# Performance work log

Measured on AMD Instinct MI355X. Metric: run time of the kernel, lower is better.

The kernel has to match this reference:

```python
import jax, jax.numpy as jnp
import numpy as np

NUM_ITER = 3
NUM_SLOTS = 8
INPUT_SIZE = 256
SLOT_SIZE = 256
MLP_HIDDEN = 512
HEADS = 4
EPSILON = 1e-8
LN_EPS = 1e-5


def _ln(x, g, b):
    m = jnp.mean(x, axis=-1, keepdims=True)
    v = jnp.mean((x - m) ** 2, axis=-1, keepdims=True)
    return (x - m) * jax.lax.rsqrt(v + LN_EPS) * g + b


def setup_inputs() -> dict:
    key = jax.random.key(0)
    ks = jax.random.split(key, 16)
    B, Nkv, Nq = 64, 1024, NUM_SLOTS
    S, D, Hm = SLOT_SIZE, INPUT_SIZE, MLP_HIDDEN
    def w(k, shape, fan_in):
        return jax.random.normal(k, shape, jnp.float32) * (fan_in ** -0.5)
    return {
        "inputs": jax.random.normal(ks[0], (B, Nkv, D), jnp.float32),
        "slots": jax.random.normal(ks[1], (B, Nq, S), jnp.float32),
        "ln_in_g": jnp.ones((D,), jnp.float32), "ln_in_b": jnp.zeros((D,), jnp.float32),
        "ln_sl_g": jnp.ones((S,), jnp.float32), "ln_sl_b": jnp.zeros((S,), jnp.float32),
        "ln_mlp_g": jnp.ones((S,), jnp.float32), "ln_mlp_b": jnp.zeros((S,), jnp.float32),
        "Wq": w(ks[2], (S, S), S),
        "Wk": w(ks[3], (D, S), D),
        "Wv": w(ks[4], (D, S), D),
        "gru_w_ih": w(ks[5], (3 * S, S), S),
        "gru_w_hh": w(ks[6], (3 * S, S), S),
        "gru_b_ih": jnp.zeros((3 * S,), jnp.float32),
        "gru_b_hh": jnp.zeros((3 * S,), jnp.float32),
        "mlp_w1": w(ks[7], (S, Hm), S),
        "mlp_b1": jnp.zeros((Hm,), jnp.float32),
        "mlp_w2": w(ks[8], (Hm, S), Hm),
        "mlp_b2": jnp.zeros((S,), jnp.float32),
    }


def reference(inputs, slots, ln_in_g, ln_in_b, ln_sl_g, ln_sl_b, ln_mlp_g, ln_mlp_b,
              Wq, Wk, Wv, gru_w_ih, gru_w_hh, gru_b_ih, gru_b_hh,
              mlp_w1, mlp_b1, mlp_w2, mlp_b2):
    B, Nkv, _ = inputs.shape
    _, Nq, S = slots.shape
    H = HEADS
    hd = S // H

    x = _ln(inputs, ln_in_g, ln_in_b)
    k = (x @ Wk).reshape(B, Nkv, H, hd).transpose(0, 2, 1, 3)  # [B,H,Nkv,hd]
    v = (x @ Wv).reshape(B, Nkv, H, hd).transpose(0, 2, 1, 3)  # [B,H,Nkv,hd]
    k = k * (hd ** -0.5)

    attn_vis = None
    for _ in range(NUM_ITER):
        slots_prev = slots
        s = _ln(slots, ln_sl_g, ln_sl_b)
        q = (s @ Wq).reshape(B, Nq, H, hd).transpose(0, 2, 1, 3)  # [B,H,Nq,hd]
        # logits [B,H,Nkv,Nq]
        logits = jnp.einsum('bhnd,bhqd->bhnq', k, q)
        # softmax over (heads * slots) jointly, per kv token
        flat = logits.transpose(0, 2, 1, 3).reshape(B, Nkv, H * Nq)
        attn = jax.nn.softmax(flat, axis=-1).reshape(B, Nkv, H, Nq).transpose(0, 2, 1, 3)
        attn_vis = attn.sum(axis=1).swapaxes(1, 2)  # [B,Nq,Nkv]
        attn = attn + EPSILON
        attn = attn / jnp.sum(attn, axis=-2, keepdims=True)  # normalize over Nkv
        updates = jnp.einsum('bhnq,bhnd->bqhd', attn, v).reshape(B, Nq, S)

        # GRU cell (torch gate order: r, z, n)
        xg = updates.reshape(-1, S) @ gru_w_ih.T + gru_b_ih
        hprev = slots_prev.reshape(-1, S)
        hg = hprev @ gru_w_hh.T + gru_b_hh
        xr, xz, xn = jnp.split(xg, 3, axis=-1)
        hr, hz, hn = jnp.split(hg, 3, axis=-1)
        r = jax.nn.sigmoid(xr + hr)
        z = jax.nn.sigmoid(xz + hz)
        n = jnp.tanh(xn + r * hn)
        h = (1.0 - z) * n + z * hprev
        slots = h.reshape(B, Nq, S)

        m = _ln(slots, ln_mlp_g, ln_mlp_b)
        slots = slots + (jax.nn.relu(m @ mlp_w1 + mlp_b1) @ mlp_w2 + mlp_b2)

    return slots, jax.lax.stop_gradient(attn_vis)
```

## Files before the change

### kernel.cpp

```cpp
#include <hip/hip_runtime.h>
#include <hip/hip_bf16.h>
#include <math.h>

#define EPS_  1e-8f
#define LNEPS 1e-5f

typedef __attribute__((ext_vector_type(8))) short   short8;
typedef __attribute__((ext_vector_type(8))) __bf16  bf16x8;
typedef __attribute__((ext_vector_type(4))) float   f32x4;
typedef unsigned short ushort_t;

__device__ __forceinline__ float bf2f(unsigned int u) { return __uint_as_float(u << 16); }
__device__ __forceinline__ unsigned short f2bf(float f) {
    unsigned int u = __float_as_uint(f);
    u += 0x7fff + ((u >> 16) & 1);
    return (unsigned short)(u >> 16);
}
__device__ __forceinline__ unsigned int cvt_pk_bf16(float lo, float hi) {
    unsigned int r;
    asm("v_cvt_pk_bf16_f32 %0, %1, %2" : "=v"(r) : "v"(lo), "v"(hi));
    return r;
}
__device__ __forceinline__ f32x4 mfma_bf16(short8 a, short8 b, f32x4 c) {
    union U { short8 s; bf16x8 b; };
    U ua, ub; ua.s = a; ub.s = b;
    return __builtin_amdgcn_mfma_f32_16x16x32_bf16(ua.b, ub.b, c, 0, 0, 0);
}
__device__ __forceinline__ float wred_sum(float v) {
#pragma unroll
    for (int off = 32; off > 0; off >>= 1) v += __shfl_xor(v, off);
    return v;
}

__global__ __launch_bounds__(256) void prepack_w_kernel(const float* __restrict__ Wk,
                                                        const float* __restrict__ Wv,
                                                        ushort_t* __restrict__ Wt) {
    int n = blockIdx.x;
    int k = threadIdx.x;
    float v = (n < 256) ? Wk[(size_t)k * 256 + n] * 0.125f : Wv[(size_t)k * 256 + (n - 256)];
    Wt[(size_t)n * 256 + k] = f2bf(v);
}

__global__ __launch_bounds__(256) void prepack_wtp_kernel(const ushort_t* __restrict__ Wt,
                                                          ushort_t* __restrict__ Wtp) {
    int bs = blockIdx.x;
    int wv = bs >> 3, s = bs & 7;
    int ni = threadIdx.x >> 6, l = threadIdx.x & 63;
    int n  = wv * 64 + ni * 16 + (l & 15);
    int k0 = s * 32 + (l >> 4) * 8;
    short8 v = *(const short8*)(Wt + (size_t)n * 256 + k0);
    *(short8*)(Wtp + ((size_t)bs * 4 + ni) * 512 + l * 8) = v;
}

__global__ __launch_bounds__(512) void prepack_slotw_kernel(const float* __restrict__ w_ih,
                                                            const float* __restrict__ w_hh,
                                                            const float* __restrict__ w1,
                                                            const float* __restrict__ w2,
                                                            const float* __restrict__ Wq,
                                                            ushort_t* __restrict__ wg,
                                                            ushort_t* __restrict__ w1p,
                                                            ushort_t* __restrict__ w2q,
                                                            ushort_t* __restrict__ Wqp) {
    int t = threadIdx.x, bid = blockIdx.x, sec = blockIdx.y;
    if (sec == 0) {
        if (bid < 256) {
            int k = bid, c = t & 255;
            const float* src = (t >> 8) ? w_hh : w_ih;
            size_t o = ((size_t)k * 512 + t) * 4;
            wg[o + 0] = f2bf(src[(size_t)(0 * 256 + c) * 256 + k]);
            wg[o + 1] = f2bf(src[(size_t)(1 * 256 + c) * 256 + k]);
            wg[o + 2] = f2bf(src[(size_t)(2 * 256 + c) * 256 + k]);
            wg[o + 3] = 0;
        }
    } else if (sec == 1) {
        if (bid < 64) {
            size_t o = ((size_t)bid * 512 + t) * 4;
#pragma unroll
            for (int i = 0; i < 4; i++) w1p[o + i] = f2bf(w1[(size_t)(bid * 4 + i) * 512 + t]);
        }
    } else if (sec == 2) {
        if (bid < 64) {
            int k4g = bid * 2 + (t >> 8), c = t & 255;
            size_t o = ((size_t)k4g * 256 + c) * 4;
#pragma unroll
            for (int i = 0; i < 4; i++) w2q[o + i] = f2bf(w2[(size_t)(k4g * 4 + i) * 256 + c]);
        }
    } else {
        if (bid < 32) {
            int k4g = bid * 2 + (t >> 8), c = t & 255;
            size_t o = ((size_t)k4g * 256 + c) * 4;
#pragma unroll
            for (int i = 0; i < 4; i++) Wqp[o + i] = f2bf(Wq[(size_t)(k4g * 4 + i) * 256 + c]);
        }
    }
}

__global__ __launch_bounds__(512, 4) void kvproj_mfma_kernel(const float* __restrict__ in,
                                                             const float* __restrict__ g,
                                                             const float* __restrict__ bb,
                                                             const ushort_t* __restrict__ Wtp,
                                                             ushort_t* __restrict__ kvout) {
    __shared__ __align__(16) ushort_t As[64 * 256];
    const int tid = threadIdx.x;
    const int wv = tid >> 6, l = tid & 63;
    const int kc = l >> 4, lr = l & 15;
    const int m0 = blockIdx.x * 64;

    float4 g4 = *(const float4*)(g + l * 4);
    float4 b4 = *(const float4*)(bb + l * 4);
    float4 xv[8];
#pragma unroll
    for (int i = 0; i < 8; i++)
        xv[i] = *(const float4*)(in + (size_t)(m0 + i * 8 + wv) * 256 + l * 4);
#pragma unroll
    for (int i = 0; i < 8; i++) {
        float s1 = xv[i].x + xv[i].y + xv[i].z + xv[i].w;
        float s2 = xv[i].x * xv[i].x + xv[i].y * xv[i].y + xv[i].z * xv[i].z + xv[i].w * xv[i].w;
        s1 = wred_sum(s1);
        s2 = wred_sum(s2);
        float m = s1 * (1.0f / 256.0f);
        float r = rsqrtf(s2 * (1.0f / 256.0f) - m * m + LNEPS);
        float v0 = (xv[i].x - m) * r * g4.x + b4.x;
        float v1 = (xv[i].y - m) * r * g4.y + b4.y;
        float v2 = (xv[i].z - m) * r * g4.z + b4.z;
        float v3 = (xv[i].w - m) * r * g4.w + b4.w;
        uint2 pk = {cvt_pk_bf16(v0, v1), cvt_pk_bf16(v2, v3)};
        int row = i * 8 + wv;
        *(uint2*)&As[row * 256 + (((l >> 1) ^ (row & 15)) * 8) + (l & 1) * 4] = pk;
    }
    __syncthreads();

    f32x4 zero = {0.f, 0.f, 0.f, 0.f};
    f32x4 acc[4][4];
#pragma unroll
    for (int i = 0; i < 4; i++)
#pragma unroll
        for (int jj = 0; jj < 4; jj++) acc[i][jj] = zero;

    const ushort_t* wbase = Wtp + ((size_t)(wv * 8) * 4) * 512 + l * 8;
    short8 bcur[4], bnxt[4];
#pragma unroll
    for (int ni = 0; ni < 4; ni++) bcur[ni] = *(const short8*)(wbase + ni * 512);

#pragma unroll
    for (int s = 0; s < 8; s++) {
        if (s < 7) {
            const ushort_t* wpb = wbase + (size_t)(s + 1) * 4 * 512;
#pragma unroll
            for (int ni = 0; ni < 4; ni++) bnxt[ni] = *(const short8*)(wpb + ni * 512);
        }
        short8 af[4];
#pragma unroll
        for (int mi = 0; mi < 4; mi++) {
            int r2 = lr + mi * 16;
            int c = s * 4 + kc;
            af[mi] = *(const short8*)&As[r2 * 256 + ((c ^ (r2 & 15)) * 8)];
        }
#pragma unroll
        for (int mi = 0; mi < 4; mi++)
#pragma unroll
            for (int ni = 0; ni < 4; ni++)
                acc[mi][ni] = mfma_bf16(af[mi], bcur[ni], acc[mi][ni]);
        if (s < 7) {
#pragma unroll
            for (int ni = 0; ni < 4; ni++) bcur[ni] = bnxt[ni];
        }
    }

    const int odd = l & 1;
    const int colbase = wv * 64;
#pragma unroll
    for (int mi = 0; mi < 4; mi++)
#pragma unroll
        for (int ni = 0; ni < 4; ni++) {
            float s0 = odd ? acc[mi][ni][0] : acc[mi][ni][2];
            float s1_ = odd ? acc[mi][ni][1] : acc[mi][ni][3];
            float r0 = __shfl_xor(s0, 1);
            float r1_ = __shfl_xor(s1_, 1);
            int col0 = colbase + ni * 16 + (lr & ~1);
            unsigned int packA, packB;
            int rowA;
            if (!odd) {
                packA = cvt_pk_bf16(acc[mi][ni][0], r0);
                packB = cvt_pk_bf16(acc[mi][ni][1], r1_);
                rowA = m0 + mi * 16 + kc * 4 + 0;
            } else {
                packA = cvt_pk_bf16(r0, acc[mi][ni][2]);
                packB = cvt_pk_bf16(r1_, acc[mi][ni][3]);
                rowA = m0 + mi * 16 + kc * 4 + 2;
            }
            *(unsigned int*)(kvout + (size_t)rowA * 512 + col0) = packA;
            *(unsigned int*)(kvout + (size_t)(rowA + 1) * 512 + col0) = packB;
        }
}

__global__ __launch_bounds__(256) void qproj_kernel(const float* __restrict__ slots,
                                                    const float* __restrict__ g,
                                                    const float* __restrict__ bvec,
                                                    const float* __restrict__ Wq,
                                                    float* __restrict__ qp) {
    int row = blockIdx.x;
    int tid = threadIdx.x;
    __shared__ float s_s[256];
    __shared__ float red[8];
    float x = slots[(size_t)row * 256 + tid];
    float s1 = wred_sum(x);
    float s2 = wred_sum(x * x);
    if ((tid & 63) == 0) { red[tid >> 6] = s1; red[4 + (tid >> 6)] = s2; }
    __syncthreads();
    float m  = (red[0] + red[1] + red[2] + red[3]) * (1.0f / 256.0f);
    float e2 = (red[4] + red[5] + red[6] + red[7]) * (1.0f / 256.0f);
    float rst = rsqrtf(e2 - m * m + LNEPS);
    s_s[tid] = (x - m) * rst * g[tid] + bvec[tid];
    __syncthreads();
    float acc = 0.f;
#pragma unroll 4
    for (int d = 0; d < 256; d++) acc += s_s[d] * Wq[(size_t)d * 256 + tid];
    int b = row >> 3, q = row & 7;
    qp[((size_t)(b * 4 + (tid >> 6)) * 8 + q) * 64 + (tid & 63)] = acc;
}

__global__ __launch_bounds__(256) void attn_fused_kernel(const ushort_t* __restrict__ kv,
                                                         const float* __restrict__ qp,
                                                         float* __restrict__ Upart,
                                                         float* __restrict__ Cpart,
                                                         float* __restrict__ vis,
                                                         int write_vis) {
    int b = blockIdx.y;
    int chunk = blockIdx.x;
    int tid = threadIdx.x;
    __shared__ __align__(16) ushort_t qfrag[16 * 512];
    __shared__ float att[128][32];
    __shared__ float ubuf[2][2048];
    __shared__ float cred[8][32];

    {
        const float* qb_ = qp + (size_t)b * 2048;
#pragma unroll
        for (int snt = 0; snt < 16; snt++) {
            int s = snt >> 1, nt = snt & 1;
#pragma unroll
            for (int rep = 0; rep < 2; rep++) {
                int idx = tid + rep * 256;
                int k  = s * 32 + ((idx >> 7) << 3) + (idx & 7);
                int hq = nt * 16 + ((idx >> 3) & 15);
                float v = ((k >> 6) == (hq >> 3))
                              ? qb_[(hq >> 3) * 512 + (hq & 7) * 64 + (k & 63)] : 0.f;
                qfrag[snt * 512 + idx] = f2bf(v);
            }
        }
    }
    __syncthreads();

    const int w = tid >> 6, l = tid & 63;
    const int lr = l & 15, kc8 = (l >> 4) * 8;

    short8 qb2[2][8];
#pragma unroll
    for (int s = 0; s < 8; s++) {
        qb2[0][s] = *(const short8*)&qfrag[(s * 2 + 0) * 512 + l * 8];
        qb2[1][s] = *(const short8*)&qfrag[(s * 2 + 1) * 512 + l * 8];
    }
    f32x4 zero = {0.f, 0.f, 0.f, 0.f};
#pragma unroll
    for (int mi_loc = 0; mi_loc < 2; mi_loc++) {
        int mi = w * 2 + mi_loc;
        f32x4 a0 = zero, a1 = zero;
        const ushort_t* abase = kv + (size_t)(b * 1024 + chunk * 128 + mi * 16 + lr) * 512 + kc8;
#pragma unroll
        for (int s = 0; s < 8; s++) {
            short8 af = *(const short8*)(abase + s * 32);
            a0 = mfma_bf16(af, qb2[0][s], a0);
            a1 = mfma_bf16(af, qb2[1][s], a1);
        }
        int row0 = mi * 16 + (l >> 4) * 4;
#pragma unroll
        for (int r = 0; r < 4; r++) {
            att[row0 + r][lr]      = a0[r];
            att[row0 + r][16 + lr] = a1[r];
        }
    }
    __syncthreads();

    {
        int token = tid >> 1, half = tid & 1;
        float v[16];
        float mx = -3.4e38f;
#pragma unroll
        for (int j = 0; j < 16; j++) { v[j] = att[token][half * 16 + j]; mx = fmaxf(mx, v[j]); }
        mx = fmaxf(mx, __shfl_xor(mx, 1));
        float sm = 0.f;
#pragma unroll
        for (int j = 0; j < 16; j++) { v[j] = __expf(v[j] - mx); sm += v[j]; }
        sm += __shfl_xor(sm, 1);
        float inv = 1.0f / sm;
#pragma unroll
        for (int j = 0; j < 16; j++) { v[j] *= inv; att[token][half * 16 + j] = v[j] + EPS_; }
        if (write_vis) {
#pragma unroll
            for (int q = 0; q < 8; q++) {
                float pv = v[q] + v[q + 8];
                float pf = pv + __shfl_xor(pv, 1);
                if (half == 0) vis[(size_t)(b * 8 + q) * 1024 + chunk * 128 + token] = pf;
            }
        }
    }
    __syncthreads();

    {
        int hq2 = tid & 31, grp = tid >> 5;
        float s = 0.f;
#pragma unroll
        for (int i = 0; i < 16; i++) s += att[grp * 16 + i][hq2];
        cred[grp][hq2] = s;
    }
    __syncthreads();
    if (tid < 32) {
        float s = 0.f;
#pragma unroll
        for (int g2 = 0; g2 < 8; g2++) s += cred[g2][tid];
        Cpart[(size_t)(b * 8 + chunk) * 32 + tid] = s;
    }

    const int h_u = l >> 4, d4 = l & 15;
    const int uo = h_u * 64 + d4 * 4;
    float U[8][4];
#pragma unroll
    for (int q = 0; q < 8; q++)
#pragma unroll
        for (int d = 0; d < 4; d++) U[q][d] = 0.f;
    const ushort_t* vbase = kv + (size_t)(b * 1024 + chunk * 128 + w * 32) * 512 + 256 + uo;
    for (int i = 0; i < 32; ++i) {
        uint2 vp = *(const uint2*)(vbase + (size_t)i * 512);
        float v0 = bf2f(vp.x & 0xffffu), v1 = bf2f(vp.x >> 16);
        float v2 = bf2f(vp.y & 0xffffu), v3 = bf2f(vp.y >> 16);
        const float* arow = &att[w * 32 + i][h_u * 8];
        float4 a01 = *(const float4*)(arow);
        float4 a23 = *(const float4*)(arow + 4);
        float aq[8] = {a01.x, a01.y, a01.z, a01.w, a23.x, a23.y, a23.z, a23.w};
#pragma unroll
        for (int q = 0; q < 8; q++) {
            U[q][0] += aq[q] * v0; U[q][1] += aq[q] * v1;
            U[q][2] += aq[q] * v2; U[q][3] += aq[q] * v3;
        }
    }
    if (w & 1) {
        float* dst = ubuf[w >> 1];
#pragma unroll
        for (int q = 0; q < 8; q++) {
            float4 uq = {U[q][0], U[q][1], U[q][2], U[q][3]};
            *(float4*)(dst + q * 256 + uo) = uq;
        }
    }
    __syncthreads();
    if (!(w & 1)) {
        const float* src = ubuf[w >> 1];
#pragma unroll
        for (int q = 0; q < 8; q++) {
            float4 uq = *(const float4*)(src + q * 256 + uo);
            U[q][0] += uq.x; U[q][1] += uq.y; U[q][2] += uq.z; U[q][3] += uq.w;
        }
    }
    __syncthreads();
    if (w == 2) {
        float* dst = ubuf[0];
#pragma unroll
        for (int q = 0; q < 8; q++) {
            float4 uq = {U[q][0], U[q][1], U[q][2], U[q][3]};
            *(float4*)(dst + q * 256 + uo) = uq;
        }
    }
    __syncthreads();
    if (w == 0) {
        const float* src = ubuf[0];
        float* up = Upart + (size_t)(b * 8 + chunk) * 2048 + uo;
#pragma unroll
        for (int q = 0; q < 8; q++) {
            float4 uq = *(const float4*)(src + q * 256 + uo);
            float4 o = {U[q][0] + uq.x, U[q][1] + uq.y, U[q][2] + uq.z, U[q][3] + uq.w};
            *(float4*)(up + q * 256) = o;
        }
    }
}

__global__ __launch_bounds__(1024) void slot_fused_kernel(const float* __restrict__ Upart,
                                                          const float* __restrict__ Cpart,
                                                          const float* __restrict__ slotsIn,
                                                          const ushort_t* __restrict__ wg,
                                                          const float* __restrict__ b_ih,
                                                          const float* __restrict__ b_hh,
                                                          const float* __restrict__ ln_mlp_g,
                                                          const float* __restrict__ ln_mlp_b,
                                                          const ushort_t* __restrict__ w1p,
                                                          const float* __restrict__ b1,
                                                          const ushort_t* __restrict__ w2q,
                                                          const float* __restrict__ b2,
                                                          const float* __restrict__ ln_sl_g,
                                                          const float* __restrict__ ln_sl_b,
                                                          const ushort_t* __restrict__ Wqp,
                                                          float* __restrict__ slotsOut,
                                                          float* __restrict__ qp,
                                                          int emit_qp) {
    __shared__ float U_s[2][256], H_s[2][256];
    __shared__ float rsum[2][2][256];
    __shared__ float gpart[2][12][256];
    __shared__ float SB_s[2][256], M_s[2][256];
    __shared__ float hid_s[2][512];
    __shared__ float mpart[2][2][512];
    __shared__ float ppart[4][2][256];
    __shared__ float redA[8], redB[8];
    const int t = threadIdx.x;
    const int kh = t >> 9, s9 = t & 511;
    const int rr = s9 >> 8, c = s9 & 255;
    const int lane = t & 63, wvi = t >> 6;
    const int r0 = blockIdx.x * 2;
    const int rg = r0 + rr, bb_ = rg >> 3, q = rg & 7;

    {
        float s = 0.f;
#pragma unroll
        for (int p2 = 0; p2 < 4; p2++)
            s += Upart[(size_t)(bb_ * 8 + kh * 4 + p2) * 2048 + q * 256 + c];
        rsum[kh][rr][c] = s;
    }
    __syncthreads();
    if (kh == 0) {
        int h = c >> 6;
        float C = 0.f;
#pragma unroll
        for (int p2 = 0; p2 < 8; p2++)
            C += Cpart[(size_t)(bb_ * 8 + p2) * 32 + h * 8 + q];
        U_s[rr][c] = (rsum[0][rr][c] + rsum[1][rr][c]) / C;
        H_s[rr][c] = slotsIn[(size_t)rg * 256 + c];
    }
    __syncthreads();

    {
        float ar0, az0, an0;
        if (kh == 0) {
            const float* bias = rr ? b_hh : b_ih;
            ar0 = bias[c]; az0 = bias[256 + c]; an0 = bias[512 + c];
        } else { ar0 = az0 = an0 = 0.f; }
        float ar1 = ar0, az1 = az0, an1 = an0;
        const float (*act)[256] = rr ? H_s : U_s;
        const ushort_t* wp = wg + (size_t)s9 * 4;
        for (int cc = 0; cc < 8; cc++) {
            uint2 wreg[16];
#pragma unroll
            for (int i = 0; i < 16; i++) {
                int k = kh * 128 + cc * 16 + i;
                wreg[i] = *(const uint2*)(wp + (size_t)k * 2048);
            }
#pragma unroll
            for (int i = 0; i < 16; i++) {
                int k = kh * 128 + cc * 16 + i;
                float w0  = bf2f(wreg[i].x & 0xffffu);
                float w1_ = bf2f(wreg[i].x >> 16);
                float w2_ = bf2f(wreg[i].y & 0xffffu);
                float a0 = act[0][k], a1 = act[1][k];
                ar0 += a0 * w0; az0 += a0 * w1_; an0 += a0 * w2_;
                ar1 += a1 * w0; az1 += a1 * w1_; an1 += a1 * w2_;
            }
        }
        gpart[kh][rr * 6 + 0][c] = ar0; gpart[kh][rr * 6 + 1][c] = ar1;
        gpart[kh][rr * 6 + 2][c] = az0; gpart[kh][rr * 6 + 3][c] = az1;
        gpart[kh][rr * 6 + 4][c] = an0; gpart[kh][rr * 6 + 5][c] = an1;
    }
    __syncthreads();

    float sb = 0.f;
    if (kh == 0) {
        float xr = gpart[0][0 + rr][c] + gpart[1][0 + rr][c];
        float xz = gpart[0][2 + rr][c] + gpart[1][2 + rr][c];
        float xn = gpart[0][4 + rr][c] + gpart[1][4 + rr][c];
        float hr = gpart[0][6 + rr][c] + gpart[1][6 + rr][c];
        float hz = gpart[0][8 + rr][c] + gpart[1][8 + rr][c];
        float hn = gpart[0][10 + rr][c] + gpart[1][10 + rr][c];
        float rg_ = 1.f / (1.f + __expf(-(xr + hr)));
        float z   = 1.f / (1.f + __expf(-(xz + hz)));
        float nn  = tanhf(xn + rg_ * hn);
        sb = (1.f - z) * nn + z * H_s[rr][c];
        SB_s[rr][c] = sb;
        float s1 = wred_sum(sb), s2 = wred_sum(sb * sb);
        if (lane == 0) { redA[wvi] = s1; redB[wvi] = s2; }
    }
    __syncthreads();
    if (kh == 0) {
        int base = rr * 4;
        float m  = (redA[base] + redA[base + 1] + redA[base + 2] + redA[base + 3]) * (1.f / 256.f);
        float e2 = (redB[base] + redB[base + 1] + redB[base + 2] + redB[base + 3]) * (1.f / 256.f);
        float rst = rsqrtf(e2 - m * m + LNEPS);
        M_s[rr][c] = (sb - m) * rst * ln_mlp_g[c] + ln_mlp_b[c];
    }
    __syncthreads();

    {
        float h10 = 0.f, h11 = 0.f;
        const ushort_t* wp = w1p + (size_t)s9 * 4;
        for (int cc = 0; cc < 2; cc++) {
            uint2 wreg[16];
#pragma unroll
            for (int i = 0; i < 16; i++) {
                int k4 = kh * 32 + cc * 16 + i;
                wreg[i] = *(const uint2*)(wp + (size_t)k4 * 2048);
            }
#pragma unroll
            for (int i = 0; i < 16; i++) {
                int k4 = kh * 32 + cc * 16 + i;
                float wA[4] = {bf2f(wreg[i].x & 0xffffu), bf2f(wreg[i].x >> 16),
                               bf2f(wreg[i].y & 0xffffu), bf2f(wreg[i].y >> 16)};
#pragma unroll
                for (int ii = 0; ii < 4; ii++) {
                    int k = k4 * 4 + ii;
                    h10 += M_s[0][k] * wA[ii];
                    h11 += M_s[1][k] * wA[ii];
                }
            }
        }
        mpart[kh][0][s9] = h10;
        mpart[kh][1][s9] = h11;
    }
    __syncthreads();
    if (kh == 0) {
        float bb1 = b1[s9];
        hid_s[0][s9] = fmaxf(mpart[0][0][s9] + mpart[1][0][s9] + bb1, 0.f);
        hid_s[1][s9] = fmaxf(mpart[0][1][s9] + mpart[1][1][s9] + bb1, 0.f);
    }
    __syncthreads();

    {
        int q2 = kh * 2 + rr;
        float p0 = 0.f, p1 = 0.f;
        const ushort_t* wp = w2q + (size_t)c * 4;
        for (int cc = 0; cc < 2; cc++) {
            uint2 wreg[16];
#pragma unroll
            for (int i = 0; i < 16; i++) {
                int k4g = q2 * 32 + cc * 16 + i;
                wreg[i] = *(const uint2*)(wp + (size_t)k4g * 1024);
            }
#pragma unroll
            for (int i = 0; i < 16; i++) {
                int k4g = q2 * 32 + cc * 16 + i;
                float wA[4] = {bf2f(wreg[i].x & 0xffffu), bf2f(wreg[i].x >> 16),
                               bf2f(wreg[i].y & 0xffffu), bf2f(wreg[i].y >> 16)};
#pragma unroll
                for (int ii = 0; ii < 4; ii++) {
                    int k = k4g * 4 + ii;
                    p0 += hid_s[0][k] * wA[ii];
                    p1 += hid_s[1][k] * wA[ii];
                }
            }
        }
        ppart[q2][0][c] = p0;
        ppart[q2][1][c] = p1;
    }
    __syncthreads();
    float outv = 0.f;
    if (kh == 0) {
        outv = ppart[0][rr][c] + ppart[1][rr][c] + ppart[2][rr][c] + ppart[3][rr][c]
             + b2[c] + SB_s[rr][c];
        slotsOut[(size_t)rg * 256 + c] = outv;
    }

    if (emit_qp) {
        __syncthreads();
        if (kh == 0) {
            float s1 = wred_sum(outv), s2 = wred_sum(outv * outv);
            if (lane == 0) { redA[wvi] = s1; redB[wvi] = s2; }
        }
        __syncthreads();
        if (kh == 0) {
            int base = rr * 4;
            float m  = (redA[base] + redA[base + 1] + redA[base + 2] + redA[base + 3]) * (1.f / 256.f);
            float e2 = (redB[base] + redB[base + 1] + redB[base + 2] + redB[base + 3]) * (1.f / 256.f);
            float rst = rsqrtf(e2 - m * m + LNEPS);
            M_s[rr][c] = (outv - m) * rst * ln_sl_g[c] + ln_sl_b[c];
        }
        __syncthreads();
        {
            int q2 = kh * 2 + rr;
            float p0 = 0.f, p1 = 0.f;
            const ushort_t* wp = Wqp + (size_t)c * 4;
            uint2 wreg[16];
#pragma unroll
            for (int i = 0; i < 16; i++) {
                int k4g = q2 * 16 + i;
                wreg[i] = *(const uint2*)(wp + (size_t)k4g * 1024);
            }
#pragma unroll
            for (int i = 0; i < 16; i++) {
                int k4g = q2 * 16 + i;
                float wA[4] = {bf2f(wreg[i].x & 0xffffu), bf2f(wreg[i].x >> 16),
                               bf2f(wreg[i].y & 0xffffu), bf2f(wreg[i].y >> 16)};
#pragma unroll
                for (int ii = 0; ii < 4; ii++) {
                    int k = k4g * 4 + ii;
                    p0 += M_s[0][k] * wA[ii];
                    p1 += M_s[1][k] * wA[ii];
                }
            }
            ppart[q2][0][c] = p0;
            ppart[q2][1][c] = p1;
        }
        __syncthreads();
        if (kh == 0) {
            float qv = ppart[0][rr][c] + ppart[1][rr][c] + ppart[2][rr][c] + ppart[3][rr][c];
            qp[(size_t)bb_ * 2048 + (c >> 6) * 512 + q * 64 + (c & 63)] = qv;
        }
    }
}

extern "C" void kernel_launch(void* const* d_in, const int* in_sizes, int n_in,
                              void* d_out, int out_size, void* d_ws, size_t ws_size,
                              hipStream_t stream) {
    const float* inputs   = (const float*)d_in[0];
    const float* slots0   = (const float*)d_in[1];
    const float* ln_in_g  = (const float*)d_in[2];
    const float* ln_in_b  = (const float*)d_in[3];
    const float* ln_sl_g  = (const float*)d_in[4];
    const float* ln_sl_b  = (const float*)d_in[5];
    const float* ln_mlp_g = (const float*)d_in[6];
    const float* ln_mlp_b = (const float*)d_in[7];
    const float* Wq       = (const float*)d_in[8];
    const float* Wk       = (const float*)d_in[9];
    const float* Wv       = (const float*)d_in[10];
    const float* w_ih     = (const float*)d_in[11];
    const float* w_hh     = (const float*)d_in[12];
    const float* b_ih     = (const float*)d_in[13];
    const float* b_hh     = (const float*)d_in[14];
    const float* w1       = (const float*)d_in[15];
    const float* b1       = (const float*)d_in[16];
    const float* w2       = (const float*)d_in[17];
    const float* b2       = (const float*)d_in[18];

    float* out_slots = (float*)d_out;
    float* out_vis   = (float*)d_out + 64 * 8 * 256;

    char* p = (char*)d_ws;
    auto carve = [&](size_t bytes) {
        void* r = (void*)p;
        p += (bytes + 255) & ~(size_t)255;
        return r;
    };
    ushort_t* kv   = (ushort_t*)carve((size_t)65536 * 512 * 2);
    ushort_t* Wt   = (ushort_t*)carve((size_t)512 * 256 * 2);
    ushort_t* Wtp  = (ushort_t*)carve((size_t)512 * 256 * 2);
    ushort_t* wg   = (ushort_t*)carve((size_t)256 * 512 * 4 * 2);
    ushort_t* w1p  = (ushort_t*)carve((size_t)64 * 512 * 4 * 2);
    ushort_t* w2q  = (ushort_t*)carve((size_t)128 * 256 * 4 * 2);
    ushort_t* Wqp  = (ushort_t*)carve((size_t)64 * 256 * 4 * 2);
    float* qp      = (float*)carve((size_t)64 * 2048 * 4);
    float* Upart   = (float*)carve((size_t)64 * 8 * 2048 * 4);
    float* Cpart   = (float*)carve((size_t)64 * 8 * 32 * 4);
    float* slotsA  = (float*)carve((size_t)512 * 256 * 4);

    prepack_w_kernel<<<512, 256, 0, stream>>>(Wk, Wv, Wt);
    prepack_wtp_kernel<<<64, 256, 0, stream>>>(Wt, Wtp);
    prepack_slotw_kernel<<<dim3(256, 4), 512, 0, stream>>>(w_ih, w_hh, w1, w2, Wq,
                                                           wg, w1p, w2q, Wqp);
    kvproj_mfma_kernel<<<1024, 512, 0, stream>>>(inputs, ln_in_g, ln_in_b, Wtp, kv);
    qproj_kernel<<<512, 256, 0, stream>>>(slots0, ln_sl_g, ln_sl_b, Wq, qp);

    for (int it = 0; it < 3; ++it) {
        attn_fused_kernel<<<dim3(8, 64), 256, 0, stream>>>(kv, qp, Upart, Cpart, out_vis,
                                                           (it == 2) ? 1 : 0);
        slot_fused_kernel<<<256, 1024, 0, stream>>>(
            Upart, Cpart, (it == 0) ? slots0 : slotsA,
            wg, b_ih, b_hh, ln_mlp_g, ln_mlp_b, w1p, b1, w2q, b2,
            ln_sl_g, ln_sl_b, Wqp,
            (it == 2) ? out_slots : slotsA, qp, (it < 2) ? 1 : 0);
    }
}
```

Baseline: 210.7 us.

## Store V transposed and compute attention-weighted V sum with MFMA

The KV projection kernel now writes K and V to separate buffers, with V stored transposed per batch (d-major over tokens). The attention kernel builds a transposed bf16 copy of the attention weights in shared memory and computes the update sums with bf16 MFMA instead of scalar FMA loops, which also removes the cross-wave reduction through shared memory and its barriers. The B-operand register double-buffering in the projection loop is dropped. In exchange, the attention weights are rounded to bf16 before the V product, and the padded zero rows add MFMA work.

```diff
diff --git a/kernel.cpp b/kernel.cpp
--- a/kernel.cpp
+++ b/kernel.cpp
@@ -99,7 +99,8 @@
                                                              const float* __restrict__ g,
                                                              const float* __restrict__ bb,
                                                              const ushort_t* __restrict__ Wtp,
-                                                             ushort_t* __restrict__ kvout) {
+                                                             ushort_t* __restrict__ kvK,
+                                                             ushort_t* __restrict__ vT) {
     __shared__ __align__(16) ushort_t As[64 * 256];
     const int tid = threadIdx.x;
     const int wv = tid >> 6, l = tid & 63;
@@ -138,17 +139,12 @@
         for (int jj = 0; jj < 4; jj++) acc[i][jj] = zero;
 
     const ushort_t* wbase = Wtp + ((size_t)(wv * 8) * 4) * 512 + l * 8;
-    short8 bcur[4], bnxt[4];
-#pragma unroll
-    for (int ni = 0; ni < 4; ni++) bcur[ni] = *(const short8*)(wbase + ni * 512);
-
 #pragma unroll
     for (int s = 0; s < 8; s++) {
-        if (s < 7) {
-            const ushort_t* wpb = wbase + (size_t)(s + 1) * 4 * 512;
-#pragma unroll
-            for (int ni = 0; ni < 4; ni++) bnxt[ni] = *(const short8*)(wpb + ni * 512);
-        }
+        short8 bfr[4];
+        const ushort_t* wpb = wbase + (size_t)s * 4 * 512;
+#pragma unroll
+        for (int ni = 0; ni < 4; ni++) bfr[ni] = *(const short8*)(wpb + ni * 512);
         short8 af[4];
 #pragma unroll
         for (int mi = 0; mi < 4; mi++) {
@@ -160,38 +156,50 @@
         for (int mi = 0; mi < 4; mi++)
 #pragma unroll
             for (int ni = 0; ni < 4; ni++)
-                acc[mi][ni] = mfma_bf16(af[mi], bcur[ni], acc[mi][ni]);
-        if (s < 7) {
-#pragma unroll
-            for (int ni = 0; ni < 4; ni++) bcur[ni] = bnxt[ni];
-        }
-    }
-
-    const int odd = l & 1;
-    const int colbase = wv * 64;
-#pragma unroll
-    for (int mi = 0; mi < 4; mi++)
-#pragma unroll
-        for (int ni = 0; ni < 4; ni++) {
-            float s0 = odd ? acc[mi][ni][0] : acc[mi][ni][2];
-            float s1_ = odd ? acc[mi][ni][1] : acc[mi][ni][3];
-            float r0 = __shfl_xor(s0, 1);
-            float r1_ = __shfl_xor(s1_, 1);
-            int col0 = colbase + ni * 16 + (lr & ~1);
-            unsigned int packA, packB;
-            int rowA;
-            if (!odd) {
-                packA = cvt_pk_bf16(acc[mi][ni][0], r0);
-                packB = cvt_pk_bf16(acc[mi][ni][1], r1_);
-                rowA = m0 + mi * 16 + kc * 4 + 0;
-            } else {
-                packA = cvt_pk_bf16(r0, acc[mi][ni][2]);
-                packB = cvt_pk_bf16(r1_, acc[mi][ni][3]);
-                rowA = m0 + mi * 16 + kc * 4 + 2;
-            }
-            *(unsigned int*)(kvout + (size_t)rowA * 512 + col0) = packA;
-            *(unsigned int*)(kvout + (size_t)(rowA + 1) * 512 + col0) = packB;
-        }
+                acc[mi][ni] = mfma_bf16(af[mi], bfr[ni], acc[mi][ni]);
+    }
+
+    if (wv < 4) {
+        const int odd = l & 1;
+        const int colbase = wv * 64;
+#pragma unroll
+        for (int mi = 0; mi < 4; mi++)
+#pragma unroll
+            for (int ni = 0; ni < 4; ni++) {
+                float s0 = odd ? acc[mi][ni][0] : acc[mi][ni][2];
+                float s1_ = odd ? acc[mi][ni][1] : acc[mi][ni][3];
+                float r0 = __shfl_xor(s0, 1);
+                float r1_ = __shfl_xor(s1_, 1);
+                int col0 = colbase + ni * 16 + (lr & ~1);
+                unsigned int packA, packB;
+                int rowA;
+                if (!odd) {
+                    packA = cvt_pk_bf16(acc[mi][ni][0], r0);
+                    packB = cvt_pk_bf16(acc[mi][ni][1], r1_);
+                    rowA = m0 + mi * 16 + kc * 4 + 0;
+                } else {
+                    packA = cvt_pk_bf16(r0, acc[mi][ni][2]);
+                    packB = cvt_pk_bf16(r1_, acc[mi][ni][3]);
+                    rowA = m0 + mi * 16 + kc * 4 + 2;
+                }
+                *(unsigned int*)(kvK + (size_t)rowA * 256 + col0) = packA;
+                *(unsigned int*)(kvK + (size_t)(rowA + 1) * 256 + col0) = packB;
+            }
+    } else {
+        const int bI = m0 >> 10;
+        const int tbase = m0 & 1023;
+#pragma unroll
+        for (int mi = 0; mi < 4; mi++)
+#pragma unroll
+            for (int ni = 0; ni < 4; ni++) {
+                int d = (wv - 4) * 64 + ni * 16 + lr;
+                int tok = tbase + mi * 16 + kc * 4;
+                uint2 pk;
+                pk.x = cvt_pk_bf16(acc[mi][ni][0], acc[mi][ni][1]);
+                pk.y = cvt_pk_bf16(acc[mi][ni][2], acc[mi][ni][3]);
+                *(uint2*)(vT + ((size_t)bI * 256 + d) * 1024 + tok) = pk;
+            }
+    }
 }
 
 __global__ __launch_bounds__(256) void qproj_kernel(const float* __restrict__ slots,
@@ -220,7 +228,8 @@
     qp[((size_t)(b * 4 + (tid >> 6)) * 8 + q) * 64 + (tid & 63)] = acc;
 }
 
-__global__ __launch_bounds__(256) void attn_fused_kernel(const ushort_t* __restrict__ kv,
+__global__ __launch_bounds__(256) void attn_fused_kernel(const ushort_t* __restrict__ kvK,
+                                                         const ushort_t* __restrict__ vT,
                                                          const float* __restrict__ qp,
                                                          float* __restrict__ Upart,
                                                          float* __restrict__ Cpart,
@@ -230,8 +239,8 @@
     int chunk = blockIdx.x;
     int tid = threadIdx.x;
     __shared__ __align__(16) ushort_t qfrag[16 * 512];
-    __shared__ float att[128][32];
-    __shared__ float ubuf[2][2048];
+    __shared__ float att[128][33];
+    __shared__ __align__(16) ushort_t attT[64][136];
     __shared__ float cred[8][32];
 
     {
@@ -249,11 +258,16 @@
                 qfrag[snt * 512 + idx] = f2bf(v);
             }
         }
+        for (int idx = tid; idx < 32 * 68; idx += 256) {
+            int z = idx / 68, j = idx - z * 68;
+            int row = (z >> 3) * 16 + 8 + (z & 7);
+            *(unsigned int*)&attT[row][j * 2] = 0u;
+        }
     }
     __syncthreads();
 
     const int w = tid >> 6, l = tid & 63;
-    const int lr = l & 15, kc8 = (l >> 4) * 8;
+    const int lr = l & 15, kc = l >> 4, kc8 = kc * 8;
 
     short8 qb2[2][8];
 #pragma unroll
@@ -266,14 +280,14 @@
     for (int mi_loc = 0; mi_loc < 2; mi_loc++) {
         int mi = w * 2 + mi_loc;
         f32x4 a0 = zero, a1 = zero;
-        const ushort_t* abase = kv + (size_t)(b * 1024 + chunk * 128 + mi * 16 + lr) * 512 + kc8;
+        const ushort_t* abase = kvK + (size_t)(b * 1024 + chunk * 128 + mi * 16 + lr) * 256 + kc8;
 #pragma unroll
         for (int s = 0; s < 8; s++) {
             short8 af = *(const short8*)(abase + s * 32);
             a0 = mfma_bf16(af, qb2[0][s], a0);
             a1 = mfma_bf16(af, qb2[1][s], a1);
         }
-        int row0 = mi * 16 + (l >> 4) * 4;
+        int row0 = mi * 16 + kc * 4;
 #pragma unroll
         for (int r = 0; r < 4; r++) {
             att[row0 + r][lr]      = a0[r];
@@ -295,11 +309,16 @@
         sm += __shfl_xor(sm, 1);
         float inv = 1.0f / sm;
 #pragma unroll
-        for (int j = 0; j < 16; j++) { v[j] *= inv; att[token][half * 16 + j] = v[j] + EPS_; }
+        for (int j = 0; j < 16; j++) {
+            v[j] = v[j] * inv + EPS_;
+            att[token][half * 16 + j] = v[j];
+            int hq = half * 16 + j;
+            attT[(hq >> 3) * 16 + (hq & 7)][token] = f2bf(v[j]);
+        }
         if (write_vis) {
 #pragma unroll
             for (int q = 0; q < 8; q++) {
-                float pv = v[q] + v[q + 8];
+                float pv = (v[q] - EPS_) + (v[q + 8] - EPS_);
                 float pf = pv + __shfl_xor(pv, 1);
                 if (half == 0) vis[(size_t)(b * 8 + q) * 1024 + chunk * 128 + token] = pf;
             }
@@ -322,63 +341,30 @@
         Cpart[(size_t)(b * 8 + chunk) * 32 + tid] = s;
     }
 
-    const int h_u = l >> 4, d4 = l & 15;
-    const int uo = h_u * 64 + d4 * 4;
-    float U[8][4];
-#pragma unroll
-    for (int q = 0; q < 8; q++)
-#pragma unroll
-        for (int d = 0; d < 4; d++) U[q][d] = 0.f;
-    const ushort_t* vbase = kv + (size_t)(b * 1024 + chunk * 128 + w * 32) * 512 + 256 + uo;
-    for (int i = 0; i < 32; ++i) {
-        uint2 vp = *(const uint2*)(vbase + (size_t)i * 512);
-        float v0 = bf2f(vp.x & 0xffffu), v1 = bf2f(vp.x >> 16);
-        float v2 = bf2f(vp.y & 0xffffu), v3 = bf2f(vp.y >> 16);
-        const float* arow = &att[w * 32 + i][h_u * 8];
-        float4 a01 = *(const float4*)(arow);
-        float4 a23 = *(const float4*)(arow + 4);
-        float aq[8] = {a01.x, a01.y, a01.z, a01.w, a23.x, a23.y, a23.z, a23.w};
-#pragma unroll
-        for (int q = 0; q < 8; q++) {
-            U[q][0] += aq[q] * v0; U[q][1] += aq[q] * v1;
-            U[q][2] += aq[q] * v2; U[q][3] += aq[q] * v3;
-        }
-    }
-    if (w & 1) {
-        float* dst = ubuf[w >> 1];
-#pragma unroll
-        for (int q = 0; q < 8; q++) {
-            float4 uq = {U[q][0], U[q][1], U[q][2], U[q][3]};
-            *(float4*)(dst + q * 256 + uo) = uq;
-        }
-    }
-    __syncthreads();
-    if (!(w & 1)) {
-        const float* src = ubuf[w >> 1];
-#pragma unroll
-        for (int q = 0; q < 8; q++) {
-            float4 uq = *(const float4*)(src + q * 256 + uo);
-            U[q][0] += uq.x; U[q][1] += uq.y; U[q][2] += uq.z; U[q][3] += uq.w;
-        }
-    }
-    __syncthreads();
-    if (w == 2) {
-        float* dst = ubuf[0];
-#pragma unroll
-        for (int q = 0; q < 8; q++) {
-            float4 uq = {U[q][0], U[q][1], U[q][2], U[q][3]};
-            *(float4*)(dst + q * 256 + uo) = uq;
-        }
-    }
-    __syncthreads();
-    if (w == 0) {
-        const float* src = ubuf[0];
-        float* up = Upart + (size_t)(b * 8 + chunk) * 2048 + uo;
-#pragma unroll
-        for (int q = 0; q < 8; q++) {
-            float4 uq = *(const float4*)(src + q * 256 + uo);
-            float4 o = {U[q][0] + uq.x, U[q][1] + uq.y, U[q][2] + uq.z, U[q][3] + uq.w};
-            *(float4*)(up + q * 256) = o;
+    {
+        const int h = w;
+        f32x4 acc[4];
+#pragma unroll
+        for (int nt = 0; nt < 4; nt++) acc[nt] = zero;
+        const ushort_t* vrow = vT + ((size_t)b * 256 + h * 64) * 1024 + chunk * 128 + kc8;
+#pragma unroll
+        for (int ks = 0; ks < 4; ks++) {
+            short8 afr = *(const short8*)&attT[h * 16 + lr][ks * 32 + kc8];
+#pragma unroll
+            for (int nt = 0; nt < 4; nt++) {
+                short8 bfr = *(const short8*)(vrow + (size_t)(nt * 16 + lr) * 1024 + ks * 32);
+                acc[nt] = mfma_bf16(afr, bfr, acc[nt]);
+            }
+        }
+        if (kc < 2) {
+            float* up = Upart + (size_t)(b * 8 + chunk) * 2048 + h * 64;
+#pragma unroll
+            for (int nt = 0; nt < 4; nt++)
+#pragma unroll
+                for (int r = 0; r < 4; r++) {
+                    int q = kc * 4 + r;
+                    up[q * 256 + nt * 16 + lr] = acc[nt][r];
+                }
         }
     }
 }
@@ -643,7 +629,8 @@
         p += (bytes + 255) & ~(size_t)255;
         return r;
     };
-    ushort_t* kv   = (ushort_t*)carve((size_t)65536 * 512 * 2);
+    ushort_t* kvK  = (ushort_t*)carve((size_t)65536 * 256 * 2);
+    ushort_t* vT   = (ushort_t*)carve((size_t)64 * 256 * 1024 * 2);
     ushort_t* Wt   = (ushort_t*)carve((size_t)512 * 256 * 2);
     ushort_t* Wtp  = (ushort_t*)carve((size_t)512 * 256 * 2);
     ushort_t* wg   = (ushort_t*)carve((size_t)256 * 512 * 4 * 2);
@@ -659,12 +646,12 @@
     prepack_wtp_kernel<<<64, 256, 0, stream>>>(Wt, Wtp);
     prepack_slotw_kernel<<<dim3(256, 4), 512, 0, stream>>>(w_ih, w_hh, w1, w2, Wq,
                                                            wg, w1p, w2q, Wqp);
-    kvproj_mfma_kernel<<<1024, 512, 0, stream>>>(inputs, ln_in_g, ln_in_b, Wtp, kv);
+    kvproj_mfma_kernel<<<1024, 512, 0, stream>>>(inputs, ln_in_g, ln_in_b, Wtp, kvK, vT);
     qproj_kernel<<<512, 256, 0, stream>>>(slots0, ln_sl_g, ln_sl_b, Wq, qp);
 
     for (int it = 0; it < 3; ++it) {
-        attn_fused_kernel<<<dim3(8, 64), 256, 0, stream>>>(kv, qp, Upart, Cpart, out_vis,
-                                                           (it == 2) ? 1 : 0);
+        attn_fused_kernel<<<dim3(8, 64), 256, 0, stream>>>(kvK, vT, qp, Upart, Cpart,
+                                                           out_vis, (it == 2) ? 1 : 0);
         slot_fused_kernel<<<256, 1024, 0, stream>>>(
             Upart, Cpart, (it == 0) ? slots0 : slotsA,
             wg, b_ih, b_hh, ln_mlp_g, ln_mlp_b, w1p, b1, w2q, b2,
```

New measurement: 211.2 us. No clear change (+0.2%).
